# Kernel optimization log

Hardware: AMD Instinct MI355X
Metric: run time of the kernel (lower is better)

The kernel has to match this reference:

```python
import jax, jax.numpy as jnp
import numpy as np

T, N, E, V, D, H, Dh = 64, 2048, 8192, 64000, 128, 12, 10  # head_size = 128 // 12 = 10


def setup_inputs() -> dict:
    key = jax.random.key(0)
    ks = jax.random.split(key, 16)
    s = 1.0 / np.sqrt(D)
    return {
        "node_ids": jax.random.randint(ks[0], (T, N), 0, V, dtype=jnp.int32),
        "src": jax.random.randint(ks[1], (T, E), 0, N, dtype=jnp.int32),
        "dst": jax.random.randint(ks[2], (T, E), 0, N, dtype=jnp.int32),
        "edge_weights": jax.random.uniform(ks[3], (T, E), dtype=jnp.float32),
        "emb": jax.random.normal(ks[4], (V, D), dtype=jnp.float32) * 0.02,
        "Wp": jax.random.normal(ks[5], (D, D), dtype=jnp.float32) * s,
        "bp": jnp.zeros((D,), jnp.float32),
        "Wq": jax.random.normal(ks[6], (D, H * Dh), dtype=jnp.float32) * s,
        "bq": jnp.zeros((H * Dh,), jnp.float32),
        "Wk": jax.random.normal(ks[7], (D, H * Dh), dtype=jnp.float32) * s,
        "bk": jnp.zeros((H * Dh,), jnp.float32),
        "Wv": jax.random.normal(ks[8], (D, H * Dh), dtype=jnp.float32) * s,
        "bv": jnp.zeros((H * Dh,), jnp.float32),
        "Wo": jax.random.normal(ks[9], (H * Dh, 2), dtype=jnp.float32) * (1.0 / np.sqrt(H * Dh)),
        "bo": jnp.zeros((2,), jnp.float32),
    }


def reference(node_ids, src, dst, edge_weights, emb, Wp, bp, Wq, bq, Wk, bk, Wv, bv, Wo, bo):
    def propagate(x, s, d, w):
        # edge-weighted gather-multiply-scatter-add, then linear projection
        msg = x[s] * w[:, None]                                   # [E, D]
        n_hat = x + jax.ops.segment_sum(msg, d, num_segments=N)   # [N, D]
        return n_hat @ Wp + bp

    def step(carry, inp):
        ids, s, d, w = inp
        x = emb[ids]                       # [N, D] embedding lookup
        x = propagate(x, s, d, w)
        x = propagate(x, s, d, w)
        x = propagate(x, s, d, w)          # three rounds, as in SpatialEncoding.forward
        return carry, x

    _, node_emb = jax.lax.scan(step, None, (node_ids, src, dst, edge_weights))  # [T, N, D]

    # per-node temporal sequence: [N, T, D]
    seq = jnp.transpose(node_emb, (1, 0, 2))

    q = (seq @ Wq + bq).reshape(N, T, H, Dh)
    k = (seq @ Wk + bk).reshape(N, T, H, Dh)
    v = (seq @ Wv + bv).reshape(N, T, H, Dh)

    scale = 1.0 / jnp.sqrt(jnp.float32(Dh))
    scores = jnp.einsum('nthd,nshd->nhts', q, k) * scale          # [N, H, T, T]
    attn = jax.nn.softmax(scores, axis=-1)
    out = jnp.einsum('nhts,nshd->nthd', attn, v).reshape(N, T, H * Dh)  # [N, T, 120]

    # agg = cat over nodes -> [N*T, 120]; transpose(1,0).mean(-1) == mean over N*T axis
    agg = out.reshape(N * T, H * Dh).mean(axis=0)                 # [120]
    return agg @ Wo + bo                                          # [2]
```

## Files before the change

### kernel.cpp

```cpp
#include <hip/hip_runtime.h>
#include <stdint.h>

#define TT 64
#define NN 2048
#define EE 8192
#define DD 128
#define CAP 32

typedef __attribute__((ext_vector_type(8))) short bvec8;
typedef __attribute__((ext_vector_type(4))) float fvec4;

__device__ __forceinline__ float bf2f(uint16_t u){
  union { uint32_t i; float f; } v; v.i = ((uint32_t)u) << 16; return v.f;
}
__device__ __forceinline__ uint16_t f2bf(float f){
  union { float f; uint32_t i; } v; v.f = f;
  uint32_t r = v.i + 0x7fffu + ((v.i >> 16) & 1u);
  return (uint16_t)(r >> 16);
}
__device__ __forceinline__ uint32_t cvtpk(float lo, float hi){
  uint32_t r;
  asm("v_cvt_pk_bf16_f32 %0, %1, %2" : "=v"(r) : "v"(lo), "v"(hi));
  return r;
}
__device__ __forceinline__ fvec4 mfma16(bvec8 a, bvec8 b, fvec4 c){
  return __builtin_amdgcn_mfma_f32_16x16x32_bf16(a, b, c, 0, 0, 0);
}
__device__ __forceinline__ bvec8 pack8z(float a, float b, float c, float d){
  union { uint32_t u[4]; bvec8 v; } r;
  r.u[0] = cvtpk(a, b);
  r.u[1] = cvtpk(c, d);
  r.u[2] = 0u;
  r.u[3] = 0u;
  return r.v;
}

__global__ void k_fill(const int* __restrict__ dst, int* __restrict__ cnt, int* __restrict__ esw){
  int tid = blockIdx.x * 256 + threadIdx.x;
  int t = tid >> 13, e = tid & (EE - 1);
  int d = dst[tid];
  int row = t * NN + d;
  int pos = atomicAdd(&cnt[row], 1);
  if (pos < CAP) esw[(size_t)row * 2 * CAP + 2 * pos] = e;
}

__global__ void k_sortconv(int* __restrict__ cnt, int* __restrict__ esw,
                           const int* __restrict__ srcA, const float* __restrict__ ewA){
  int row = blockIdx.x * 256 + threadIdx.x;
  if (row >= TT * NN) return;
  int t = row >> 11;
  int c = cnt[row]; if (c > CAP) c = CAP;
  cnt[row] = c;
  int* p = esw + (size_t)row * 2 * CAP;
  for (int i = 0; i < c; ++i){
    int mi = i, mv = p[2 * i];
    for (int j = i + 1; j < c; ++j){ int vj = p[2 * j]; if (vj < mv){ mv = vj; mi = j; } }
    if (mi != i){ p[2 * mi] = p[2 * i]; p[2 * i] = mv; }
  }
  const int* srcT = srcA + (size_t)t * EE;
  const float* ewT = ewA + (size_t)t * EE;
  for (int i = 0; i < c; ++i){
    int e = p[2 * i];
    p[2 * i]     = srcT[e];
    p[2 * i + 1] = __float_as_int(ewT[e]);
  }
}

__global__ void k_prep(const float* __restrict__ Wp, const float* __restrict__ Wq,
                       const float* __restrict__ Wk, const float* __restrict__ Wv,
                       const float* __restrict__ bq, const float* __restrict__ bk,
                       const float* __restrict__ bv,
                       uint16_t* __restrict__ WpHi, uint16_t* __restrict__ WpLo,
                       uint16_t* __restrict__ QHi, float* __restrict__ biasPad){
  int tid = blockIdx.x * 256 + threadIdx.x;
  if (tid < 2048){
    int lane = tid & 63, kc = (tid >> 6) & 3, ct = tid >> 8;
    int g = lane >> 4, l15 = lane & 15;
    #pragma unroll
    for (int j = 0; j < 8; ++j){
      int k = kc * 32 + g * 8 + j;
      int col = ct * 16 + l15;
      float v = Wp[k * DD + col];
      uint16_t h = f2bf(v);
      WpHi[(size_t)tid * 8 + j] = h;
      WpLo[(size_t)tid * 8 + j] = f2bf(v - bf2f(h));
    }
  } else if (tid < 2048 + 9216){
    int idx = tid - 2048;
    int lane = idx & 63, kc = (idx >> 6) & 3, t2 = idx >> 8;
    int h = t2 % 12, m = t2 / 12;
    const float* W = (m == 0) ? Wq : (m == 1) ? Wk : Wv;
    int g = lane >> 4, l15 = lane & 15;
    #pragma unroll
    for (int j = 0; j < 8; ++j){
      int k = kc * 32 + g * 8 + j;
      float v = (l15 < 10) ? W[k * 120 + h * 10 + l15] : 0.f;
      QHi[(size_t)idx * 8 + j] = f2bf(v);
    }
  } else if (tid < 2048 + 9216 + 576){
    int idx = tid - (2048 + 9216);
    int m = idx / 192, rest = idx % 192;
    int h = rest / 16, d = rest % 16;
    const float* B = (m == 0) ? bq : (m == 1) ? bk : bv;
    biasPad[idx] = (d < 10) ? B[h * 10 + d] : 0.f;
  }
}

__global__ void k_gather(const int* __restrict__ ids, const float* __restrict__ emb,
                         uint16_t* __restrict__ x){
  int tid = blockIdx.x * 256 + threadIdx.x;
  int row = tid >> 4, c8 = tid & 15;
  int id = ids[row];
  const float* er = emb + (size_t)id * DD + c8 * 8;
  float4 a = *(const float4*)er;
  float4 b = *(const float4*)(er + 4);
  union { uint32_t u[4]; bvec8 v; } o;
  o.u[0] = cvtpk(a.x, a.y);
  o.u[1] = cvtpk(a.z, a.w);
  o.u[2] = cvtpk(b.x, b.y);
  o.u[3] = cvtpk(b.z, b.w);
  *(bvec8*)(x + (size_t)row * DD + c8 * 8) = o.v;
}

__global__ __launch_bounds__(256, 4) void k_prop(const uint16_t* __restrict__ xin,
    uint16_t* __restrict__ xout, const int* __restrict__ cnt, const int* __restrict__ esw,
    const uint16_t* __restrict__ WHi, const uint16_t* __restrict__ WLo,
    const float* __restrict__ bp, int topt){
  __shared__ uint16_t lds[64 * 136];
  int vb = blockIdx.x;
  int b = ((vb & 7) << 8) | (vb >> 3);
  int t = b >> 5, n0 = (b & 31) << 6;
  int tid = threadIdx.x, w = tid >> 6, lane = tid & 63, g = lane >> 4, l15 = lane & 15;
  const uint16_t* xt = xin + (size_t)t * NN * DD;
  int baseRow = t * NN + n0 + w * 16;
  int myc = (lane < 16) ? cnt[baseRow + lane] : 0;
  #pragma unroll 2
  for (int i = 0; i < 16; ++i){
    int r = w * 16 + i;
    int n = n0 + r;
    int rowg = baseRow + i;
    uint32_t u = *(const uint32_t*)(xt + (size_t)n * DD + (lane << 1));
    int c = __shfl(myc, i);
    const int4* ep = (const int4*)(esw + (size_t)rowg * 2 * CAP);
    int4 q0 = ep[0], q1 = ep[1], q2 = ep[2], q3 = ep[3];
    int sj[8]   = {q0.x, q0.z, q1.x, q1.z, q2.x, q2.z, q3.x, q3.z};
    float wj[8] = {__int_as_float(q0.y), __int_as_float(q0.w),
                   __int_as_float(q1.y), __int_as_float(q1.w),
                   __int_as_float(q2.y), __int_as_float(q2.w),
                   __int_as_float(q3.y), __int_as_float(q3.w)};
    uint32_t xs[8];
    float wf[8];
    #pragma unroll
    for (int j = 0; j < 8; ++j){
      int s = (j < c) ? sj[j] : n;
      wf[j] = (j < c) ? wj[j] : 0.f;
      xs[j] = *(const uint32_t*)(xt + (size_t)s * DD + (lane << 1));
    }
    float a0 = bf2f((uint16_t)(u & 0xffffu));
    float a1 = bf2f((uint16_t)(u >> 16));
    #pragma unroll
    for (int j = 0; j < 8; ++j){
      a0 = fmaf(wf[j], bf2f((uint16_t)(xs[j] & 0xffffu)), a0);
      a1 = fmaf(wf[j], bf2f((uint16_t)(xs[j] >> 16)), a1);
    }
    if (c > 8){
      for (int j = 8; j < c; ++j){
        int s = esw[(size_t)rowg * 2 * CAP + 2 * j];
        float wt = __int_as_float(esw[(size_t)rowg * 2 * CAP + 2 * j + 1]);
        uint32_t us = *(const uint32_t*)(xt + (size_t)s * DD + (lane << 1));
        a0 = fmaf(wt, bf2f((uint16_t)(us & 0xffffu)), a0);
        a1 = fmaf(wt, bf2f((uint16_t)(us >> 16)), a1);
      }
    }
    *(uint32_t*)&lds[r * 136 + (lane << 1)] = cvtpk(a0, a1);
  }
  __syncthreads();
  bvec8 afr[4];
  int arow = w * 16 + l15;
  #pragma unroll
  for (int kc = 0; kc < 4; ++kc)
    afr[kc] = *(const bvec8*)&lds[arow * 136 + kc * 32 + g * 8];
  fvec4 acc[8];
  #pragma unroll
  for (int i = 0; i < 8; ++i) acc[i] = fvec4{0.f, 0.f, 0.f, 0.f};
  #pragma unroll
  for (int kc = 0; kc < 4; ++kc){
    #pragma unroll
    for (int ct = 0; ct < 8; ++ct){
      size_t base = ((size_t)(ct * 4 + kc) * 64 + lane) * 8;
      acc[ct] = mfma16(afr[kc], *(const bvec8*)&WHi[base], acc[ct]);
      acc[ct] = mfma16(afr[kc], *(const bvec8*)&WLo[base], acc[ct]);
    }
  }
  __syncthreads();
  #pragma unroll
  for (int ct = 0; ct < 8; ++ct){
    int col = ct * 16 + l15;
    float bias = bp[col];
    uint32_t c01 = cvtpk(acc[ct][0] + bias, acc[ct][1] + bias);
    uint32_t c23 = cvtpk(acc[ct][2] + bias, acc[ct][3] + bias);
    int r = w * 16 + g * 4;
    lds[(r + 0) * 136 + col] = (uint16_t)c01;
    lds[(r + 1) * 136 + col] = (uint16_t)(c01 >> 16);
    lds[(r + 2) * 136 + col] = (uint16_t)c23;
    lds[(r + 3) * 136 + col] = (uint16_t)(c23 >> 16);
  }
  __syncthreads();
  #pragma unroll
  for (int p = 0; p < 4; ++p){
    int chunk = p * 256 + tid, r = chunk >> 4, c8 = chunk & 15;
    bvec8 v = *(const bvec8*)&lds[r * 136 + c8 * 8];
    size_t dstoff;
    if (topt == 0) dstoff = ((size_t)t * NN + n0 + r) * DD + c8 * 8;
    else           dstoff = (((size_t)(n0 + r)) * TT + t) * DD + c8 * 8;
    *(bvec8*)(xout + dstoff) = v;
  }
}

__global__ __launch_bounds__(256, 3) void k_attn(const uint16_t* __restrict__ x3,
    const uint16_t* __restrict__ QHi, const float* __restrict__ biasPad,
    float* __restrict__ partials){
  __shared__ uint16_t seq[64 * 136];
  int n = blockIdx.x;
  int tid = threadIdx.x, w = tid >> 6, lane = tid & 63, g = lane >> 4, l15 = lane & 15;
  const uint16_t* xr = x3 + (size_t)n * TT * DD;
  #pragma unroll
  for (int p4 = 0; p4 < 4; ++p4){
    int chunk = p4 * 256 + tid, r = chunk >> 4, c8 = chunk & 15;
    *(bvec8*)&seq[r * 136 + c8 * 8] = *(const bvec8*)&xr[r * 128 + c8 * 8];
  }
  __syncthreads();

  const float CSC = 0.31622776601683794f * 1.4426950408889634f;

  for (int pass = 0; pass < 3; ++pass){
    int h = pass * 4 + w;
    bvec8 qf8[4], kf8[4], vf8[4];
    #pragma unroll
    for (int m = 0; m < 3; ++m){
      fvec4 acc[4];
      #pragma unroll
      for (int i = 0; i < 4; ++i) acc[i] = fvec4{0.f, 0.f, 0.f, 0.f};
      #pragma unroll
      for (int kc = 0; kc < 4; ++kc){
        bvec8 B = *(const bvec8*)&QHi[((size_t)((m * 12 + h) * 4 + kc) * 64 + lane) * 8];
        #pragma unroll
        for (int tb = 0; tb < 4; ++tb){
          bvec8 a = *(const bvec8*)&seq[(tb * 16 + l15) * 136 + kc * 32 + g * 8];
          if (m == 2) acc[tb] = mfma16(a, B, acc[tb]);
          else        acc[tb] = mfma16(B, a, acc[tb]);
        }
      }
      if (m == 2){
        float bias = biasPad[(2 * 12 + h) * 16 + l15];
        #pragma unroll
        for (int tb = 0; tb < 4; ++tb)
          vf8[tb] = pack8z(acc[tb][0] + bias, acc[tb][1] + bias,
                           acc[tb][2] + bias, acc[tb][3] + bias);
      } else {
        float4 b4 = *(const float4*)&biasPad[(m * 12 + h) * 16 + g * 4];
        #pragma unroll
        for (int tb = 0; tb < 4; ++tb){
          bvec8 f = pack8z(acc[tb][0] + b4.x, acc[tb][1] + b4.y,
                           acc[tb][2] + b4.z, acc[tb][3] + b4.w);
          if (m == 0) qf8[tb] = f; else kf8[tb] = f;
        }
      }
    }
    float csum = 0.f;
    #pragma unroll
    for (int tb = 0; tb < 4; ++tb){
      fvec4 p[4];
      #pragma unroll
      for (int sb = 0; sb < 4; ++sb)
        p[sb] = mfma16(kf8[sb], qf8[tb], fvec4{0.f, 0.f, 0.f, 0.f});
      float s = 0.f;
      #pragma unroll
      for (int sb = 0; sb < 4; ++sb)
        #pragma unroll
        for (int rg = 0; rg < 4; ++rg){
          float pv = exp2f(fminf(p[sb][rg] * CSC, 80.0f));
          p[sb][rg] = pv;
          s += pv;
        }
      s += __shfl_xor(s, 16);
      s += __shfl_xor(s, 32);
      float rinv = __builtin_amdgcn_rcpf(s);
      fvec4 o = fvec4{0.f, 0.f, 0.f, 0.f};
      #pragma unroll
      for (int sb = 0; sb < 4; ++sb){
        bvec8 pf = pack8z(p[sb][0] * rinv, p[sb][1] * rinv,
                          p[sb][2] * rinv, p[sb][3] * rinv);
        o = mfma16(pf, vf8[sb], o);
      }
      csum += o[0] + o[1] + o[2] + o[3];
    }
    csum += __shfl_xor(csum, 16);
    csum += __shfl_xor(csum, 32);
    if (g == 0 && l15 < 10)
      partials[(size_t)n * 120 + h * 10 + l15] = csum;
  }
}

__global__ void k_reduce(const float* __restrict__ partials, float* __restrict__ agg){
  __shared__ float red[256];
  int c = blockIdx.x, tid = threadIdx.x;
  float s = 0.f;
  for (int b = tid; b < NN; b += 256) s += partials[(size_t)b * 120 + c];
  red[tid] = s;
  __syncthreads();
  for (int st = 128; st > 0; st >>= 1){
    if (tid < st) red[tid] += red[tid + st];
    __syncthreads();
  }
  if (tid == 0) agg[c] = red[0] * (1.0f / (float)(NN * TT));
}

__global__ void k_final(const float* __restrict__ agg, const float* __restrict__ Wo,
                        const float* __restrict__ bo, float* __restrict__ out){
  __shared__ float r0[128], r1[128];
  int j = threadIdx.x;
  float a = (j < 120) ? agg[j] : 0.f;
  r0[j] = (j < 120) ? a * Wo[2 * j] : 0.f;
  r1[j] = (j < 120) ? a * Wo[2 * j + 1] : 0.f;
  __syncthreads();
  for (int st = 64; st > 0; st >>= 1){
    if (j < st){ r0[j] += r0[j + st]; r1[j] += r1[j + st]; }
    __syncthreads();
  }
  if (j == 0){ out[0] = r0[0] + bo[0]; out[1] = r1[0] + bo[1]; }
}

extern "C" void kernel_launch(void* const* d_in, const int* in_sizes, int n_in,
                              void* d_out, int out_size, void* d_ws, size_t ws_size,
                              hipStream_t stream){
  const int*   node_ids = (const int*)d_in[0];
  const int*   srcA     = (const int*)d_in[1];
  const int*   dstA     = (const int*)d_in[2];
  const float* ew       = (const float*)d_in[3];
  const float* emb      = (const float*)d_in[4];
  const float* Wp       = (const float*)d_in[5];
  const float* bp       = (const float*)d_in[6];
  const float* Wq       = (const float*)d_in[7];
  const float* bq       = (const float*)d_in[8];
  const float* Wk       = (const float*)d_in[9];
  const float* bk       = (const float*)d_in[10];
  const float* Wv       = (const float*)d_in[11];
  const float* bv       = (const float*)d_in[12];
  const float* Wo       = (const float*)d_in[13];
  const float* bo       = (const float*)d_in[14];

  char* p = (char*)d_ws;
  auto alloc = [&](size_t bytes) -> char* {
    char* r = p; p += (bytes + 255) & ~(size_t)255; return r;
  };
  uint16_t* xA    = (uint16_t*)alloc((size_t)TT * NN * DD * 2);
  uint16_t* xB    = (uint16_t*)alloc((size_t)TT * NN * DD * 2);
  int*      cnt   = (int*)alloc((size_t)TT * NN * 4);
  int*      esw   = (int*)alloc((size_t)TT * NN * 2 * CAP * 4);
  uint16_t* WpHi  = (uint16_t*)alloc(2048 * 8 * 2);
  uint16_t* WpLo  = (uint16_t*)alloc(2048 * 8 * 2);
  uint16_t* QHi   = (uint16_t*)alloc(9216 * 8 * 2);
  float*    biasP = (float*)alloc(576 * 4);
  float*    parts = (float*)alloc((size_t)NN * 120 * 4);
  float*    agg   = (float*)alloc(120 * 4);

  hipMemsetAsync(cnt, 0, (size_t)TT * NN * 4, stream);
  k_fill<<<TT * EE / 256, 256, 0, stream>>>(dstA, cnt, esw);
  k_sortconv<<<TT * NN / 256, 256, 0, stream>>>(cnt, esw, srcA, ew);
  k_prep<<<47, 256, 0, stream>>>(Wp, Wq, Wk, Wv, bq, bk, bv, WpHi, WpLo, QHi, biasP);
  k_gather<<<TT * NN * 16 / 256, 256, 0, stream>>>(node_ids, emb, xA);
  k_prop<<<2048, 256, 0, stream>>>(xA, xB, cnt, esw, WpHi, WpLo, bp, 0);
  k_prop<<<2048, 256, 0, stream>>>(xB, xA, cnt, esw, WpHi, WpLo, bp, 0);
  k_prop<<<2048, 256, 0, stream>>>(xA, xB, cnt, esw, WpHi, WpLo, bp, 1);
  k_attn<<<NN, 256, 0, stream>>>(xB, QHi, biasP, parts);
  k_reduce<<<120, 256, 0, stream>>>(parts, agg);
  k_final<<<1, 128, 0, stream>>>(agg, Wo, bo, (float*)d_out);
}
```

Before: 290.3 us.

## Merge setup kernels, stage edge lists in LDS, batch gathers, prescale queries

The edge-fill, weight-prep and embedding-gather kernels become one launch that dispatches work by block index, removing two launches and their serialization. In the propagation kernel, each block loads the first 8 edge entries of its 64 rows into LDS once. The gather loop then issues loads for 4 rows at a time to raise memory-level parallelism, at the cost of more registers. In attention, the softmax scale is folded into Q before the bf16 pack and the fminf clamp before exp2 is dropped, which removes per-score work but loses the overflow guard and slightly changes rounding.

```diff
diff --git a/kernel.cpp b/kernel.cpp
--- a/kernel.cpp
+++ b/kernel.cpp
@@ -12,6 +12,12 @@
 
 __device__ __forceinline__ float bf2f(uint16_t u){
   union { uint32_t i; float f; } v; v.i = ((uint32_t)u) << 16; return v.f;
+}
+__device__ __forceinline__ float lo16(uint32_t u){
+  union { uint32_t i; float f; } v; v.i = u << 16; return v.f;
+}
+__device__ __forceinline__ float hi16(uint32_t u){
+  union { uint32_t i; float f; } v; v.i = u & 0xffff0000u; return v.f;
 }
 __device__ __forceinline__ uint16_t f2bf(float f){
   union { float f; uint32_t i; } v; v.f = f;
@@ -35,13 +41,71 @@
   return r.v;
 }
 
-__global__ void k_fill(const int* __restrict__ dst, int* __restrict__ cnt, int* __restrict__ esw){
-  int tid = blockIdx.x * 256 + threadIdx.x;
-  int t = tid >> 13, e = tid & (EE - 1);
-  int d = dst[tid];
-  int row = t * NN + d;
-  int pos = atomicAdd(&cnt[row], 1);
-  if (pos < CAP) esw[(size_t)row * 2 * CAP + 2 * pos] = e;
+__global__ void k_init(const int* __restrict__ dst, int* __restrict__ cnt,
+                       int* __restrict__ esw,
+                       const float* __restrict__ Wp, const float* __restrict__ Wq,
+                       const float* __restrict__ Wk, const float* __restrict__ Wv,
+                       const float* __restrict__ bq, const float* __restrict__ bk,
+                       const float* __restrict__ bv,
+                       uint16_t* __restrict__ WpHi, uint16_t* __restrict__ WpLo,
+                       uint16_t* __restrict__ QHi, float* __restrict__ biasPad,
+                       const int* __restrict__ ids, const float* __restrict__ emb,
+                       uint16_t* __restrict__ x){
+  int bid = blockIdx.x;
+  if (bid < 2048){
+    int tid = bid * 256 + threadIdx.x;
+    int t = tid >> 13, e = tid & (EE - 1);
+    int d = dst[tid];
+    int row = t * NN + d;
+    int pos = atomicAdd(&cnt[row], 1);
+    if (pos < CAP) esw[(size_t)row * 2 * CAP + 2 * pos] = e;
+  } else if (bid < 2048 + 47){
+    int tid = (bid - 2048) * 256 + threadIdx.x;
+    if (tid < 2048){
+      int lane = tid & 63, kc = (tid >> 6) & 3, ct = tid >> 8;
+      int g = lane >> 4, l15 = lane & 15;
+      #pragma unroll
+      for (int j = 0; j < 8; ++j){
+        int k = kc * 32 + g * 8 + j;
+        int col = ct * 16 + l15;
+        float v = Wp[k * DD + col];
+        uint16_t h = f2bf(v);
+        WpHi[(size_t)tid * 8 + j] = h;
+        WpLo[(size_t)tid * 8 + j] = f2bf(v - bf2f(h));
+      }
+    } else if (tid < 2048 + 9216){
+      int idx = tid - 2048;
+      int lane = idx & 63, kc = (idx >> 6) & 3, t2 = idx >> 8;
+      int h = t2 % 12, m = t2 / 12;
+      const float* W = (m == 0) ? Wq : (m == 1) ? Wk : Wv;
+      int g = lane >> 4, l15 = lane & 15;
+      #pragma unroll
+      for (int j = 0; j < 8; ++j){
+        int k = kc * 32 + g * 8 + j;
+        float v = (l15 < 10) ? W[k * 120 + h * 10 + l15] : 0.f;
+        QHi[(size_t)idx * 8 + j] = f2bf(v);
+      }
+    } else if (tid < 2048 + 9216 + 576){
+      int idx = tid - (2048 + 9216);
+      int m = idx / 192, rest = idx % 192;
+      int h = rest / 16, d = rest % 16;
+      const float* B = (m == 0) ? bq : (m == 1) ? bk : bv;
+      biasPad[idx] = (d < 10) ? B[h * 10 + d] : 0.f;
+    }
+  } else {
+    int tid = (bid - 2095) * 256 + threadIdx.x;
+    int row = tid >> 4, c8 = tid & 15;
+    int id = ids[row];
+    const float* er = emb + (size_t)id * DD + c8 * 8;
+    float4 a = *(const float4*)er;
+    float4 b = *(const float4*)(er + 4);
+    union { uint32_t u[4]; bvec8 v; } o;
+    o.u[0] = cvtpk(a.x, a.y);
+    o.u[1] = cvtpk(a.z, a.w);
+    o.u[2] = cvtpk(b.x, b.y);
+    o.u[3] = cvtpk(b.z, b.w);
+    *(bvec8*)(x + (size_t)row * DD + c8 * 8) = o.v;
+  }
 }
 
 __global__ void k_sortconv(int* __restrict__ cnt, int* __restrict__ esw,
@@ -66,113 +130,67 @@
   }
 }
 
-__global__ void k_prep(const float* __restrict__ Wp, const float* __restrict__ Wq,
-                       const float* __restrict__ Wk, const float* __restrict__ Wv,
-                       const float* __restrict__ bq, const float* __restrict__ bk,
-                       const float* __restrict__ bv,
-                       uint16_t* __restrict__ WpHi, uint16_t* __restrict__ WpLo,
-                       uint16_t* __restrict__ QHi, float* __restrict__ biasPad){
-  int tid = blockIdx.x * 256 + threadIdx.x;
-  if (tid < 2048){
-    int lane = tid & 63, kc = (tid >> 6) & 3, ct = tid >> 8;
-    int g = lane >> 4, l15 = lane & 15;
-    #pragma unroll
-    for (int j = 0; j < 8; ++j){
-      int k = kc * 32 + g * 8 + j;
-      int col = ct * 16 + l15;
-      float v = Wp[k * DD + col];
-      uint16_t h = f2bf(v);
-      WpHi[(size_t)tid * 8 + j] = h;
-      WpLo[(size_t)tid * 8 + j] = f2bf(v - bf2f(h));
-    }
-  } else if (tid < 2048 + 9216){
-    int idx = tid - 2048;
-    int lane = idx & 63, kc = (idx >> 6) & 3, t2 = idx >> 8;
-    int h = t2 % 12, m = t2 / 12;
-    const float* W = (m == 0) ? Wq : (m == 1) ? Wk : Wv;
-    int g = lane >> 4, l15 = lane & 15;
-    #pragma unroll
-    for (int j = 0; j < 8; ++j){
-      int k = kc * 32 + g * 8 + j;
-      float v = (l15 < 10) ? W[k * 120 + h * 10 + l15] : 0.f;
-      QHi[(size_t)idx * 8 + j] = f2bf(v);
-    }
-  } else if (tid < 2048 + 9216 + 576){
-    int idx = tid - (2048 + 9216);
-    int m = idx / 192, rest = idx % 192;
-    int h = rest / 16, d = rest % 16;
-    const float* B = (m == 0) ? bq : (m == 1) ? bk : bv;
-    biasPad[idx] = (d < 10) ? B[h * 10 + d] : 0.f;
-  }
-}
-
-__global__ void k_gather(const int* __restrict__ ids, const float* __restrict__ emb,
-                         uint16_t* __restrict__ x){
-  int tid = blockIdx.x * 256 + threadIdx.x;
-  int row = tid >> 4, c8 = tid & 15;
-  int id = ids[row];
-  const float* er = emb + (size_t)id * DD + c8 * 8;
-  float4 a = *(const float4*)er;
-  float4 b = *(const float4*)(er + 4);
-  union { uint32_t u[4]; bvec8 v; } o;
-  o.u[0] = cvtpk(a.x, a.y);
-  o.u[1] = cvtpk(a.z, a.w);
-  o.u[2] = cvtpk(b.x, b.y);
-  o.u[3] = cvtpk(b.z, b.w);
-  *(bvec8*)(x + (size_t)row * DD + c8 * 8) = o.v;
-}
-
 __global__ __launch_bounds__(256, 4) void k_prop(const uint16_t* __restrict__ xin,
     uint16_t* __restrict__ xout, const int* __restrict__ cnt, const int* __restrict__ esw,
     const uint16_t* __restrict__ WHi, const uint16_t* __restrict__ WLo,
     const float* __restrict__ bp, int topt){
   __shared__ uint16_t lds[64 * 136];
+  __shared__ int4 eplds[256];
   int vb = blockIdx.x;
   int b = ((vb & 7) << 8) | (vb >> 3);
   int t = b >> 5, n0 = (b & 31) << 6;
   int tid = threadIdx.x, w = tid >> 6, lane = tid & 63, g = lane >> 4, l15 = lane & 15;
   const uint16_t* xt = xin + (size_t)t * NN * DD;
-  int baseRow = t * NN + n0 + w * 16;
-  int myc = (lane < 16) ? cnt[baseRow + lane] : 0;
-  #pragma unroll 2
-  for (int i = 0; i < 16; ++i){
-    int r = w * 16 + i;
-    int n = n0 + r;
-    int rowg = baseRow + i;
-    uint32_t u = *(const uint32_t*)(xt + (size_t)n * DD + (lane << 1));
-    int c = __shfl(myc, i);
-    const int4* ep = (const int4*)(esw + (size_t)rowg * 2 * CAP);
-    int4 q0 = ep[0], q1 = ep[1], q2 = ep[2], q3 = ep[3];
-    int sj[8]   = {q0.x, q0.z, q1.x, q1.z, q2.x, q2.z, q3.x, q3.z};
-    float wj[8] = {__int_as_float(q0.y), __int_as_float(q0.w),
-                   __int_as_float(q1.y), __int_as_float(q1.w),
-                   __int_as_float(q2.y), __int_as_float(q2.w),
-                   __int_as_float(q3.y), __int_as_float(q3.w)};
-    uint32_t xs[8];
-    float wf[8];
-    #pragma unroll
-    for (int j = 0; j < 8; ++j){
-      int s = (j < c) ? sj[j] : n;
-      wf[j] = (j < c) ? wj[j] : 0.f;
-      xs[j] = *(const uint32_t*)(xt + (size_t)s * DD + (lane << 1));
-    }
-    float a0 = bf2f((uint16_t)(u & 0xffffu));
-    float a1 = bf2f((uint16_t)(u >> 16));
-    #pragma unroll
-    for (int j = 0; j < 8; ++j){
-      a0 = fmaf(wf[j], bf2f((uint16_t)(xs[j] & 0xffffu)), a0);
-      a1 = fmaf(wf[j], bf2f((uint16_t)(xs[j] >> 16)), a1);
-    }
-    if (c > 8){
-      for (int j = 8; j < c; ++j){
-        int s = esw[(size_t)rowg * 2 * CAP + 2 * j];
-        float wt = __int_as_float(esw[(size_t)rowg * 2 * CAP + 2 * j + 1]);
-        uint32_t us = *(const uint32_t*)(xt + (size_t)s * DD + (lane << 1));
-        a0 = fmaf(wt, bf2f((uint16_t)(us & 0xffffu)), a0);
-        a1 = fmaf(wt, bf2f((uint16_t)(us >> 16)), a1);
-      }
-    }
-    *(uint32_t*)&lds[r * 136 + (lane << 1)] = cvtpk(a0, a1);
+  int baseRow = t * NN + n0;
+  eplds[tid] = ((const int4*)(esw + (size_t)(baseRow + (tid >> 2)) * 2 * CAP))[tid & 3];
+  int myc = (lane < 16) ? cnt[baseRow + w * 16 + lane] : 0;
+  __syncthreads();
+  for (int gi = 0; gi < 4; ++gi){
+    int rb = w * 16 + gi * 4;
+    uint32_t u4[4], xs[4][8];
+    float wfv[4][8];
+    #pragma unroll
+    for (int i = 0; i < 4; ++i)
+      u4[i] = *(const uint32_t*)(xt + (size_t)(n0 + rb + i) * DD + (lane << 1));
+    #pragma unroll
+    for (int i = 0; i < 4; ++i){
+      int c = __shfl(myc, gi * 4 + i);
+      const int4* epr = &eplds[(rb + i) * 4];
+      int4 q0 = epr[0], q1 = epr[1], q2 = epr[2], q3 = epr[3];
+      int sj[8]   = {q0.x, q0.z, q1.x, q1.z, q2.x, q2.z, q3.x, q3.z};
+      float wj[8] = {__int_as_float(q0.y), __int_as_float(q0.w),
+                     __int_as_float(q1.y), __int_as_float(q1.w),
+                     __int_as_float(q2.y), __int_as_float(q2.w),
+                     __int_as_float(q3.y), __int_as_float(q3.w)};
+      #pragma unroll
+      for (int j = 0; j < 8; ++j){
+        int s = (j < c) ? sj[j] : 0;
+        wfv[i][j] = (j < c) ? wj[j] : 0.f;
+        xs[i][j] = *(const uint32_t*)(xt + (size_t)s * DD + (lane << 1));
+      }
+    }
+    #pragma unroll
+    for (int i = 0; i < 4; ++i){
+      float a0 = lo16(u4[i]);
+      float a1 = hi16(u4[i]);
+      #pragma unroll
+      for (int j = 0; j < 8; ++j){
+        a0 = fmaf(wfv[i][j], lo16(xs[i][j]), a0);
+        a1 = fmaf(wfv[i][j], hi16(xs[i][j]), a1);
+      }
+      int c = __shfl(myc, gi * 4 + i);
+      if (c > 8){
+        int rowg = baseRow + rb + i;
+        for (int j = 8; j < c; ++j){
+          int s = esw[(size_t)rowg * 2 * CAP + 2 * j];
+          float wt = __int_as_float(esw[(size_t)rowg * 2 * CAP + 2 * j + 1]);
+          uint32_t us = *(const uint32_t*)(xt + (size_t)s * DD + (lane << 1));
+          a0 = fmaf(wt, lo16(us), a0);
+          a1 = fmaf(wt, hi16(us), a1);
+        }
+      }
+      *(uint32_t*)&lds[(rb + i) * 136 + (lane << 1)] = cvtpk(a0, a1);
+    }
   }
   __syncthreads();
   bvec8 afr[4];
@@ -251,20 +269,24 @@
           else        acc[tb] = mfma16(B, a, acc[tb]);
         }
       }
-      if (m == 2){
+      if (m == 0){
+        float4 b4 = *(const float4*)&biasPad[(0 * 12 + h) * 16 + g * 4];
+        #pragma unroll
+        for (int tb = 0; tb < 4; ++tb)
+          qf8[tb] = pack8z((acc[tb][0] + b4.x) * CSC, (acc[tb][1] + b4.y) * CSC,
+                           (acc[tb][2] + b4.z) * CSC, (acc[tb][3] + b4.w) * CSC);
+      } else if (m == 1){
+        float4 b4 = *(const float4*)&biasPad[(1 * 12 + h) * 16 + g * 4];
+        #pragma unroll
+        for (int tb = 0; tb < 4; ++tb)
+          kf8[tb] = pack8z(acc[tb][0] + b4.x, acc[tb][1] + b4.y,
+                           acc[tb][2] + b4.z, acc[tb][3] + b4.w);
+      } else {
         float bias = biasPad[(2 * 12 + h) * 16 + l15];
         #pragma unroll
         for (int tb = 0; tb < 4; ++tb)
           vf8[tb] = pack8z(acc[tb][0] + bias, acc[tb][1] + bias,
                            acc[tb][2] + bias, acc[tb][3] + bias);
-      } else {
-        float4 b4 = *(const float4*)&biasPad[(m * 12 + h) * 16 + g * 4];
-        #pragma unroll
-        for (int tb = 0; tb < 4; ++tb){
-          bvec8 f = pack8z(acc[tb][0] + b4.x, acc[tb][1] + b4.y,
-                           acc[tb][2] + b4.z, acc[tb][3] + b4.w);
-          if (m == 0) qf8[tb] = f; else kf8[tb] = f;
-        }
       }
     }
     float csum = 0.f;
@@ -279,7 +301,7 @@
       for (int sb = 0; sb < 4; ++sb)
         #pragma unroll
         for (int rg = 0; rg < 4; ++rg){
-          float pv = exp2f(fminf(p[sb][rg] * CSC, 80.0f));
+          float pv = exp2f(p[sb][rg]);
           p[sb][rg] = pv;
           s += pv;
         }
@@ -366,10 +388,10 @@
   float*    agg   = (float*)alloc(120 * 4);
 
   hipMemsetAsync(cnt, 0, (size_t)TT * NN * 4, stream);
-  k_fill<<<TT * EE / 256, 256, 0, stream>>>(dstA, cnt, esw);
+  k_init<<<2048 + 47 + 8192, 256, 0, stream>>>(dstA, cnt, esw,
+      Wp, Wq, Wk, Wv, bq, bk, bv, WpHi, WpLo, QHi, biasP,
+      node_ids, emb, xA);
   k_sortconv<<<TT * NN / 256, 256, 0, stream>>>(cnt, esw, srcA, ew);
-  k_prep<<<47, 256, 0, stream>>>(Wp, Wq, Wk, Wv, bq, bk, bv, WpHi, WpLo, QHi, biasP);
-  k_gather<<<TT * NN * 16 / 256, 256, 0, stream>>>(node_ids, emb, xA);
   k_prop<<<2048, 256, 0, stream>>>(xA, xB, cnt, esw, WpHi, WpLo, bp, 0);
   k_prop<<<2048, 256, 0, stream>>>(xB, xA, cnt, esw, WpHi, WpLo, bp, 0);
   k_prop<<<2048, 256, 0, stream>>>(xA, xB, cnt, esw, WpHi, WpLo, bp, 1);
```

Result: slower. 437.1 us (+50.6%).
